# Performance work log

Hardware: AMD Instinct MI355X
Metric: run time of the kernel (lower is better)

The kernel has to match this reference:

```python
import jax, jax.numpy as jnp
import numpy as np

NA, NB, C = 50000, 50000, 128
E = 800000
S, IN, H, NBASES = 8, 64, 64, 8
NUM_LAYERS = 2
EPS = 1e-5


def setup_inputs() -> dict:
    key = jax.random.key(0)
    ks = jax.random.split(key, 16)
    inp = {
        'x_a': jax.random.normal(ks[0], (NA, C), jnp.float32),
        'x_b': jax.random.normal(ks[1], (NB, C), jnp.float32),
        'schema_x': jax.random.normal(ks[2], (S, IN), jnp.float32),
        'edge_ab': jax.random.randint(ks[3], (2, E), 0, NA, jnp.int32),
        'edge_ba': jax.random.randint(ks[4], (2, E), 0, NA, jnp.int32),
        'edge_aa': jax.random.randint(ks[5], (2, E), 0, NA, jnp.int32),
        'schema_edge_index': jax.random.randint(ks[6], (2, 24), 0, S, jnp.int32),
        'pre_W': jax.random.normal(ks[7], (H, IN), jnp.float32) * (1.0 / np.sqrt(IN)),
        'pre_b': jnp.zeros((H,), jnp.float32),
        'gcn_W': jax.random.normal(ks[8], (H, H), jnp.float32) * (1.0 / np.sqrt(H)),
        'gcn_b': jnp.zeros((H,), jnp.float32),
        'coeff_W': jax.random.normal(ks[9], (NBASES, 2 * H), jnp.float32) * (1.0 / np.sqrt(2 * H)),
        'coeff_b': jnp.zeros((NBASES,), jnp.float32),
        'bases': jax.random.normal(ks[10], (NUM_LAYERS, NBASES, C, C), jnp.float32) * (1.0 / np.sqrt(C)),
        'sage_bias': jnp.zeros((NUM_LAYERS, 3, C), jnp.float32),
        'ln_w': jnp.ones((NUM_LAYERS, 2, C), jnp.float32),
        'ln_b': jnp.zeros((NUM_LAYERS, 2, C), jnp.float32),
    }
    return inp


def _gcn_conv(x, ei, W, b):
    # PyG GCNConv: add self-loops, symmetric normalization, then linear.
    n = x.shape[0]
    loop = jnp.arange(n, dtype=ei.dtype)
    src = jnp.concatenate([ei[0], loop])
    dst = jnp.concatenate([ei[1], loop])
    deg = jax.ops.segment_sum(jnp.ones_like(dst, jnp.float32), dst, num_segments=n)
    dinv = jax.lax.rsqrt(jnp.maximum(deg, 1e-12))
    norm = dinv[src] * dinv[dst]  # [E+n]
    xw = x @ W.T  # [n, H]
    out = jax.ops.segment_sum(xw[src] * norm[:, None], dst, num_segments=n)
    return out + b


def _sage_conv(x_src, x_dst, ei, W, b):
    # PyG SAGEConv, aggr='mean': lin_l(mean_j x_src[j]) + lin_r(x_dst); lin_l.weight == lin_r.weight == W.
    n_dst = x_dst.shape[0]
    msg_sum = jax.ops.segment_sum(x_src[ei[0]], ei[1], num_segments=n_dst)
    cnt = jax.ops.segment_sum(jnp.ones(ei.shape[1], x_src.dtype), ei[1], num_segments=n_dst)
    mean = msg_sum / jnp.maximum(cnt, 1.0)[:, None]
    return (mean + x_dst) @ W.T + b


def _layer_norm(x, w, b):
    mu = jnp.mean(x, axis=-1, keepdims=True)
    var = jnp.mean(jnp.square(x - mu), axis=-1, keepdims=True)
    return (x - mu) * jax.lax.rsqrt(var + EPS) * w + b


def _edge_weight(sf_src, sf_dst, coeff_W, coeff_b, bases_l):
    combined = jnp.concatenate([sf_src, sf_dst], axis=0)  # [2H]
    coeffs = combined @ coeff_W.T + coeff_b  # [NBASES]
    return jnp.einsum('i,ijk->jk', coeffs, bases_l)  # [C, C]


def reference(x_a, x_b, schema_x, edge_ab, edge_ba, edge_aa, schema_edge_index,
              pre_W, pre_b, gcn_W, gcn_b, coeff_W, coeff_b, bases,
              sage_bias, ln_w, ln_b):
    # Schema GCN over the tiny table-level graph. table_to_index: a->0, b->1.
    h = schema_x @ pre_W.T + pre_b
    ori = h
    sf = jax.nn.relu(_gcn_conv(h, schema_edge_index, gcn_W, gcn_b))  # [S, H]

    for l in range(NUM_LAYERS):
        bases_l = bases[l]
        W_ab = _edge_weight(sf[0], sf[1], coeff_W, coeff_b, bases_l)
        W_ba = _edge_weight(sf[1], sf[0], coeff_W, coeff_b, bases_l)
        W_aa = _edge_weight(sf[0], sf[0], coeff_W, coeff_b, bases_l)
        # HeteroConv(aggr='sum'): sum SAGE outputs per destination node type.
        out_b = _sage_conv(x_a, x_b, edge_ab, W_ab, sage_bias[l, 0])
        out_a = (_sage_conv(x_b, x_a, edge_ba, W_ba, sage_bias[l, 1])
                 + _sage_conv(x_a, x_a, edge_aa, W_aa, sage_bias[l, 2]))
        x_a = jax.nn.relu(_layer_norm(out_a, ln_w[l, 0], ln_b[l, 0]))
        x_b = jax.nn.relu(_layer_norm(out_b, ln_w[l, 1], ln_b[l, 1]))

    return x_a, x_b, sf, ori
```

## Files before the change

kernel.cpp:

```cpp
#include <hip/hip_runtime.h>

#define NA 50000
#define NB 50000
#define NN 50000
#define CDIM 128
#define EDGES 800000
#define SS 8
#define INDIM 64
#define HDIM 64
#define NBASES 8
#define NBUCK 98
#define BSH 9


__device__ __forceinline__ unsigned short f2bf(float f) {
    unsigned u = __float_as_uint(f);
    return (unsigned short)((u + 0x7FFFu + ((u >> 16) & 1u)) >> 16);
}

__global__ __launch_bounds__(512) void schema_kernel(
    const float* __restrict__ schema_x, const int* __restrict__ sei,
    const float* __restrict__ preW, const float* __restrict__ preb,
    const float* __restrict__ gcnW, const float* __restrict__ gcnb,
    const float* __restrict__ coW, const float* __restrict__ cob,
    float* __restrict__ out_sf, float* __restrict__ out_ori,
    float* __restrict__ coeffs)
{
    __shared__ float h[SS][HDIM];
    __shared__ float xw[SS][HDIM];
    __shared__ float sf[SS][HDIM];
    __shared__ float deg[SS];
    __shared__ float nrm[32];
    __shared__ int es[32], ed[32];

    int t = threadIdx.x;
    int i = t >> 6, j = t & 63;

    float acc = preb[j];
    for (int k = 0; k < INDIM; k++) acc += schema_x[i * INDIM + k] * preW[j * INDIM + k];
    h[i][j] = acc;
    out_ori[i * HDIM + j] = acc;
    if (t < SS) deg[t] = 0.0f;
    __syncthreads();

    if (t < 32) {
        int s, d;
        if (t < 24) { s = sei[t]; d = sei[24 + t]; }
        else        { s = t - 24; d = t - 24; }
        es[t] = s; ed[t] = d;
        atomicAdd(&deg[d], 1.0f);
    }
    __syncthreads();
    if (t < 32) {
        nrm[t] = rsqrtf(fmaxf(deg[es[t]], 1e-12f)) * rsqrtf(fmaxf(deg[ed[t]], 1e-12f));
    }
    float a2 = 0.0f;
    for (int k = 0; k < HDIM; k++) a2 += h[i][k] * gcnW[j * HDIM + k];
    xw[i][j] = a2;
    __syncthreads();

    float o = gcnb[j];
    for (int e = 0; e < 32; e++) {
        if (ed[e] == i) o += xw[es[e]][j] * nrm[e];
    }
    float s = fmaxf(o, 0.0f);
    sf[i][j] = s;
    out_sf[i * HDIM + j] = s;
    __syncthreads();

    if (t < 24) {
        int ty = t >> 3, ii = t & 7;
        int srow = (ty == 1) ? 1 : 0;
        int drow = (ty == 0) ? 1 : 0;
        float a = cob[ii];
        for (int k = 0; k < HDIM; k++) a += sf[srow][k] * coW[ii * (2 * HDIM) + k];
        for (int k = 0; k < HDIM; k++) a += sf[drow][k] * coW[ii * (2 * HDIM) + HDIM + k];
        coeffs[ty * 8 + ii] = a;
    }
}

__global__ __launch_bounds__(256) void build_w_kernel(
    const float* __restrict__ bases, const float* __restrict__ coeffs,
    float* __restrict__ W)
{
    int idx = blockIdx.x * blockDim.x + threadIdx.x;
    int lt = idx >> 14;
    int jk = idx & 16383;
    int j = jk >> 7, k = jk & 127;
    int l = lt / 3, ty = lt % 3;
    float acc = 0.0f;
#pragma unroll
    for (int i = 0; i < NBASES; i++)
        acc += coeffs[ty * 8 + i] * bases[((size_t)(l * NBASES + i) << 14) + jk];
    W[(lt << 14) + ((k >> 2) << 9) + (j << 2) + (k & 3)] = acc;
}

__global__ __launch_bounds__(256) void tobf16_kernel(
    const float* __restrict__ in, unsigned short* __restrict__ out, int n)
{
    int i = (blockIdx.x * 256 + threadIdx.x) * 4;
    if (i >= n) return;
    float4 f = *(const float4*)(in + i);
    ushort4 o;
    o.x = f2bf(f.x); o.y = f2bf(f.y); o.z = f2bf(f.z); o.w = f2bf(f.w);
    *(ushort4*)(out + i) = o;
}

__global__ __launch_bounds__(256) void zero_rows_kernel(
    unsigned short* a0, unsigned short* b0, unsigned short* a1, unsigned short* b1)
{
    int t = threadIdx.x;
    int tab = t >> 6, w = t & 63;
    unsigned short* p = (tab == 0) ? a0 : (tab == 1) ? b0 : (tab == 2) ? a1 : b1;
    ((unsigned*)(p + (size_t)NN * CDIM))[w] = 0u;
}


__global__ __launch_bounds__(256) void bucket_count_kernel(
    const int* __restrict__ ab, const int* __restrict__ ba,
    const int* __restrict__ aa, int* __restrict__ bcnt)
{
    __shared__ int h[NBUCK];
    int t = threadIdx.x;
    int ty = blockIdx.y;
    const int* ei = (ty == 0) ? ab : (ty == 1) ? ba : aa;
    if (t < NBUCK) h[t] = 0;
    __syncthreads();
    int cb = blockIdx.x * 4096;
    int en = min(cb + 4096, EDGES);
    for (int e = cb + t; e < en; e += 256)
        atomicAdd(&h[ei[EDGES + e] >> BSH], 1);
    __syncthreads();
    if (t < NBUCK) atomicAdd(&bcnt[ty * NBUCK + t], h[t]);
}

__global__ __launch_bounds__(32) void bucket_scan_kernel(
    const int* __restrict__ bcnt, int* __restrict__ boff, int* __restrict__ bcur)
{
    int t = threadIdx.x;
    if (t < 3) {
        int run = 0;
        for (int i = 0; i < NBUCK; i++) {
            int c = bcnt[t * NBUCK + i];
            boff[t * (NBUCK + 1) + i] = run;
            bcur[t * NBUCK + i] = run;
            run += c;
        }
        boff[t * (NBUCK + 1) + NBUCK] = run;
    }
}

__global__ __launch_bounds__(256) void bucket_partition_kernel(
    const int* __restrict__ ab, const int* __restrict__ ba,
    const int* __restrict__ aa, int* __restrict__ bcur,
    unsigned* __restrict__ buf)
{
    __shared__ int h[NBUCK];
    __shared__ int basearr[NBUCK];
    __shared__ int cur[NBUCK];
    int t = threadIdx.x;
    int ty = blockIdx.y;
    const int* ei = (ty == 0) ? ab : (ty == 1) ? ba : aa;
    if (t < NBUCK) h[t] = 0;
    __syncthreads();
    int cb = blockIdx.x * 4096;
    int en = min(cb + 4096, EDGES);
    for (int e = cb + t; e < en; e += 256)
        atomicAdd(&h[ei[EDGES + e] >> BSH], 1);
    __syncthreads();
    if (t < NBUCK) {
        basearr[t] = atomicAdd(&bcur[ty * NBUCK + t], h[t]);
        cur[t] = 0;
    }
    __syncthreads();
    for (int e = cb + t; e < en; e += 256) {
        int src = ei[e], dst = ei[EDGES + e];
        int b = dst >> BSH;
        int r = atomicAdd(&cur[b], 1);
        buf[(size_t)ty * EDGES + basearr[b] + r] =
            ((unsigned)(dst & 511) << 16) | (unsigned)src;
    }
}

__global__ __launch_bounds__(256) void bucket_scatter_kernel(
    const unsigned* __restrict__ buf, const int* __restrict__ boff,
    int* __restrict__ rowptr, int* __restrict__ col)
{
    __shared__ int cnt[512];
    __shared__ int part[256];
    int t = threadIdx.x;
    int b = blockIdx.x, ty = blockIdx.y;
    int nstart = boff[ty * (NBUCK + 1) + b];
    int nend   = boff[ty * (NBUCK + 1) + b + 1];
    int n = nend - nstart;
    cnt[t] = 0; cnt[t + 256] = 0;
    __syncthreads();
    const unsigned* bb = buf + (size_t)ty * EDGES + nstart;
    for (int i = t; i < n; i += 256)
        atomicAdd(&cnt[bb[i] >> 16], 1);
    __syncthreads();
    int a0 = cnt[2 * t], a1 = cnt[2 * t + 1];
    int s = a0 + a1;
    part[t] = s;
    __syncthreads();
    for (int off = 1; off < 256; off <<= 1) {
        int v = (t >= off) ? part[t - off] : 0;
        __syncthreads();
        part[t] += v;
        __syncthreads();
    }
    int excl = part[t] - s;
    int p0 = excl, p1 = excl + a0;
    cnt[2 * t] = p0; cnt[2 * t + 1] = p1;
    int row0 = (b << BSH) + 2 * t;
    int rbase = ty * (NN + 1);
    if (row0 < NN)     rowptr[rbase + row0] = nstart + p0;
    if (row0 + 1 < NN) rowptr[rbase + row0 + 1] = nstart + p1;
    if (b == NBUCK - 1 && t == 255) rowptr[rbase + NN] = EDGES;
    __syncthreads();
    int* cc = col + (size_t)ty * EDGES + nstart;
    for (int i = t; i < n; i += 256) {
        unsigned pk = bb[i];
        int r = atomicAdd(&cnt[pk >> 16], 1);
        cc[r] = (int)(pk & 0xFFFFu);
    }
}


__device__ __forceinline__ float4 gather2_bf(
    const unsigned short* __restrict__ xsrc, const int* __restrict__ col,
    int s, int e, int half, int off)
{
    float4 g = {0.f, 0.f, 0.f, 0.f};
    int n = e - s;
    if (n > 0) {
        int cs[16];
#pragma unroll
        for (int j = 0; j < 16; j++) {
            int slot = s + 2 * j + half;
            int cc = col[min(slot, e - 1)];
            cs[j] = (slot < e) ? cc : NN;
        }
        uint2 v[16];
#pragma unroll
        for (int j = 0; j < 8; j++)
            v[j] = *(const uint2*)(xsrc + (size_t)cs[j] * CDIM + off);
        if (n > 16) {
#pragma unroll
            for (int j = 8; j < 16; j++)
                v[j] = *(const uint2*)(xsrc + (size_t)cs[j] * CDIM + off);
        } else {
#pragma unroll
            for (int j = 8; j < 16; j++) v[j] = make_uint2(0u, 0u);
        }
#pragma unroll
        for (int j = 0; j < 16; j++) {
            g.x += __uint_as_float(v[j].x << 16);
            g.y += __uint_as_float(v[j].x & 0xffff0000u);
            g.z += __uint_as_float(v[j].y << 16);
            g.w += __uint_as_float(v[j].y & 0xffff0000u);
        }
        for (int b2 = s + 32; b2 < e; b2 += 16) {
#pragma unroll
            for (int j = 0; j < 8; j++) {
                int slot = b2 + 2 * j + half;
                int cc = col[min(slot, e - 1)];
                int id = (slot < e) ? cc : NN;
                uint2 vv = *(const uint2*)(xsrc + (size_t)id * CDIM + off);
                g.x += __uint_as_float(vv.x << 16);
                g.y += __uint_as_float(vv.x & 0xffff0000u);
                g.z += __uint_as_float(vv.y << 16);
                g.w += __uint_as_float(vv.y & 0xffff0000u);
            }
        }
    }
    g.x += __shfl_xor(g.x, 32, 64);
    g.y += __shfl_xor(g.y, 32, 64);
    g.z += __shfl_xor(g.z, 32, 64);
    g.w += __shfl_xor(g.w, 32, 64);
    return g;
}

__global__ __launch_bounds__(128) void fuse_b_kernel(
    const unsigned short* __restrict__ xsrc, const float* __restrict__ xdst,
    const int* __restrict__ rowptr, const int* __restrict__ col,
    const float* __restrict__ W, const float* __restrict__ bias,
    const float* __restrict__ lnw, const float* __restrict__ lnb,
    float* __restrict__ xnext, unsigned short* __restrict__ xnext_bf)
{
    const int R = 8;
    __shared__ __align__(16) float U[R][CDIM];
    int t = threadIdx.x;
    int base = blockIdx.x * R;
    int wv = t >> 6;
    int lane = t & 63;
    int half = lane >> 5, cl = lane & 31;
    int off = cl << 2;

    for (int rr = 0; rr < R / 2; rr++) {
        int r = rr * 2 + wv;
        int row = base + r;
        int s = rowptr[row], e = rowptr[row + 1];
        float4 g = gather2_bf(xsrc, col, s, e, half, off);
        if (half == 0) {
            float inv = 1.0f / (float)max(e - s, 1);
            float4 xv = *(const float4*)(xdst + (size_t)row * CDIM + off);
            float4 u;
            u.x = g.x * inv + xv.x; u.y = g.y * inv + xv.y;
            u.z = g.z * inv + xv.z; u.w = g.w * inv + xv.w;
            *(float4*)&U[r][off] = u;
        }
    }
    __syncthreads();

    float acc[R];
    float b = bias[t];
#pragma unroll
    for (int r = 0; r < R; r++) acc[r] = b;

    const float4* Wp4 = (const float4*)W;
    for (int k4 = 0; k4 < 32; k4++) {
        float4 w = Wp4[k4 * 128 + t];
#pragma unroll
        for (int r = 0; r < R; r++) {
            float4 u = *(const float4*)&U[r][k4 * 4];
            acc[r] += u.x * w.x + u.y * w.y + u.z * w.z + u.w * w.w;
        }
    }

    __syncthreads();
#pragma unroll
    for (int r = 0; r < R; r++) U[r][t] = acc[r];
    __syncthreads();

    float lw0 = lnw[lane], lw1 = lnw[lane + 64];
    float lb0 = lnb[lane], lb1 = lnb[lane + 64];
    for (int rr = 0; rr < R / 2; rr++) {
        int r = rr * 2 + wv;
        int row = base + r;
        float v0 = U[r][lane], v1 = U[r][lane + 64];
        float s = v0 + v1, s2 = v0 * v0 + v1 * v1;
#pragma unroll
        for (int o2 = 32; o2 > 0; o2 >>= 1) {
            s  += __shfl_xor(s,  o2, 64);
            s2 += __shfl_xor(s2, o2, 64);
        }
        float mu = s * (1.0f / CDIM);
        float var = s2 * (1.0f / CDIM) - mu * mu;
        float rs = rsqrtf(var + 1e-5f);
        float o0 = fmaxf((v0 - mu) * rs * lw0 + lb0, 0.0f);
        float o1 = fmaxf((v1 - mu) * rs * lw1 + lb1, 0.0f);
        size_t oi = (size_t)row * CDIM;
        xnext[oi + lane] = o0;
        xnext[oi + lane + 64] = o1;
        if (xnext_bf) {
            xnext_bf[oi + lane] = f2bf(o0);
            xnext_bf[oi + lane + 64] = f2bf(o1);
        }
    }
}

__global__ __launch_bounds__(128) void fuse_a_kernel(
    const unsigned short* __restrict__ xsrc1, const int* __restrict__ rowptr1, const int* __restrict__ col1,
    const unsigned short* __restrict__ xsrc2, const int* __restrict__ rowptr2, const int* __restrict__ col2,
    const float* __restrict__ xdst,
    const float* __restrict__ W1, const float* __restrict__ W2,
    const float* __restrict__ bias1, const float* __restrict__ bias2,
    const float* __restrict__ lnw, const float* __restrict__ lnb,
    float* __restrict__ xnext, unsigned short* __restrict__ xnext_bf)
{
    const int R = 8;
    __shared__ __align__(16) float U[R][CDIM];
    __shared__ __align__(16) float V[R][CDIM];
    int t = threadIdx.x;
    int base = blockIdx.x * R;
    int wv = t >> 6;
    int lane = t & 63;
    int half = lane >> 5, cl = lane & 31;
    int off = cl << 2;

    for (int rr = 0; rr < R / 2; rr++) {
        int r = rr * 2 + wv;
        int row = base + r;
        int s1 = rowptr1[row], e1 = rowptr1[row + 1];
        float4 g1 = gather2_bf(xsrc1, col1, s1, e1, half, off);
        int s2 = rowptr2[row], e2 = rowptr2[row + 1];
        float4 g2 = gather2_bf(xsrc2, col2, s2, e2, half, off);
        if (half == 0) {
            float4 xv = *(const float4*)(xdst + (size_t)row * CDIM + off);
            float i1 = 1.0f / (float)max(e1 - s1, 1);
            float i2 = 1.0f / (float)max(e2 - s2, 1);
            float4 u, v;
            u.x = g1.x * i1 + xv.x; u.y = g1.y * i1 + xv.y;
            u.z = g1.z * i1 + xv.z; u.w = g1.w * i1 + xv.w;
            v.x = g2.x * i2 + xv.x; v.y = g2.y * i2 + xv.y;
            v.z = g2.z * i2 + xv.z; v.w = g2.w * i2 + xv.w;
            *(float4*)&U[r][off] = u;
            *(float4*)&V[r][off] = v;
        }
    }
    __syncthreads();

    float acc[R];
    float b = bias1[t] + bias2[t];
#pragma unroll
    for (int r = 0; r < R; r++) acc[r] = b;

    const float4* W1p = (const float4*)W1;
    const float4* W2p = (const float4*)W2;
    for (int k4 = 0; k4 < 32; k4++) {
        float4 w1 = W1p[k4 * 128 + t];
        float4 w2 = W2p[k4 * 128 + t];
#pragma unroll
        for (int r = 0; r < R; r++) {
            float4 u = *(const float4*)&U[r][k4 * 4];
            float4 v = *(const float4*)&V[r][k4 * 4];
            acc[r] += u.x * w1.x + u.y * w1.y + u.z * w1.z + u.w * w1.w
                    + v.x * w2.x + v.y * w2.y + v.z * w2.z + v.w * w2.w;
        }
    }

    __syncthreads();
#pragma unroll
    for (int r = 0; r < R; r++) U[r][t] = acc[r];
    __syncthreads();

    float lw0 = lnw[lane], lw1 = lnw[lane + 64];
    float lb0 = lnb[lane], lb1 = lnb[lane + 64];
    for (int rr = 0; rr < R / 2; rr++) {
        int r = rr * 2 + wv;
        int row = base + r;
        float v0 = U[r][lane], v1 = U[r][lane + 64];
        float s = v0 + v1, s2 = v0 * v0 + v1 * v1;
#pragma unroll
        for (int o2 = 32; o2 > 0; o2 >>= 1) {
            s  += __shfl_xor(s,  o2, 64);
            s2 += __shfl_xor(s2, o2, 64);
        }
        float mu = s * (1.0f / CDIM);
        float var = s2 * (1.0f / CDIM) - mu * mu;
        float rs = rsqrtf(var + 1e-5f);
        float o0 = fmaxf((v0 - mu) * rs * lw0 + lb0, 0.0f);
        float o1 = fmaxf((v1 - mu) * rs * lw1 + lb1, 0.0f);
        size_t oi = (size_t)row * CDIM;
        xnext[oi + lane] = o0;
        xnext[oi + lane + 64] = o1;
        if (xnext_bf) {
            xnext_bf[oi + lane] = f2bf(o0);
            xnext_bf[oi + lane + 64] = f2bf(o1);
        }
    }
}

extern "C" void kernel_launch(void* const* d_in, const int* in_sizes, int n_in,
                              void* d_out, int out_size, void* d_ws, size_t ws_size,
                              hipStream_t stream)
{
    const float* x_a      = (const float*)d_in[0];
    const float* x_b      = (const float*)d_in[1];
    const float* schema_x = (const float*)d_in[2];
    const int*   e_ab     = (const int*)d_in[3];
    const int*   e_ba     = (const int*)d_in[4];
    const int*   e_aa     = (const int*)d_in[5];
    const int*   sei      = (const int*)d_in[6];
    const float* preW     = (const float*)d_in[7];
    const float* preb     = (const float*)d_in[8];
    const float* gcnW     = (const float*)d_in[9];
    const float* gcnb     = (const float*)d_in[10];
    const float* coW      = (const float*)d_in[11];
    const float* cob      = (const float*)d_in[12];
    const float* bases    = (const float*)d_in[13];
    const float* sbias    = (const float*)d_in[14];
    const float* lnw      = (const float*)d_in[15];
    const float* lnb      = (const float*)d_in[16];

    float* out     = (float*)d_out;
    float* out_xa  = out;
    float* out_xb  = out + 6400000;
    float* out_sf  = out + 12800000;
    float* out_ori = out + 12800512;

    float* ws = (float*)d_ws;
    int*      col    = (int*)ws;
    int*      rowptr = (int*)(ws + 2400000);
    unsigned* buf    = (unsigned*)(ws + 2550016);
    int*      bcnt   = (int*)(ws + 4950016);
    int*      boff   = (int*)(ws + 4950320);
    int*      bcur   = (int*)(ws + 4950624);
    float* xa_buf = ws + 4950928;
    float* xb_buf = ws + 11350928;
    float* Wbuf   = ws + 17750928;
    float* coeffs = ws + 17849232;
    unsigned short* xa_bf0 = (unsigned short*)(ws + 17849264);
    unsigned short* xb_bf0 = (unsigned short*)(ws + 21049328);
    unsigned short* xa_bf1 = (unsigned short*)(ws + 24249392);
    unsigned short* xb_bf1 = (unsigned short*)(ws + 27449456);

    schema_kernel<<<1, 512, 0, stream>>>(schema_x, sei, preW, preb, gcnW, gcnb,
                                         coW, cob, out_sf, out_ori, coeffs);
    build_w_kernel<<<384, 256, 0, stream>>>(bases, coeffs, Wbuf);

    tobf16_kernel<<<(NA * CDIM / 4 + 255) / 256, 256, 0, stream>>>(x_a, xa_bf0, NA * CDIM);
    tobf16_kernel<<<(NB * CDIM / 4 + 255) / 256, 256, 0, stream>>>(x_b, xb_bf0, NB * CDIM);
    zero_rows_kernel<<<1, 256, 0, stream>>>(xa_bf0, xb_bf0, xa_bf1, xb_bf1);

    hipMemsetAsync(bcnt, 0, 3 * NBUCK * sizeof(int), stream);
    dim3 cgrid((EDGES + 4095) / 4096, 3);
    bucket_count_kernel<<<cgrid, 256, 0, stream>>>(e_ab, e_ba, e_aa, bcnt);
    bucket_scan_kernel<<<1, 32, 0, stream>>>(bcnt, boff, bcur);
    bucket_partition_kernel<<<cgrid, 256, 0, stream>>>(e_ab, e_ba, e_aa, bcur, buf);
    dim3 sgrid(NBUCK, 3);
    bucket_scatter_kernel<<<sgrid, 256, 0, stream>>>(buf, boff, rowptr, col);

    const int* rp_ab = rowptr;
    const int* rp_ba = rowptr + (NN + 1);
    const int* rp_aa = rowptr + 2 * (NN + 1);
    const int* col_ab = col;
    const int* col_ba = col + EDGES;
    const int* col_aa = col + 2 * EDGES;

    for (int l = 0; l < 2; l++) {
        const float* xa_cur = (l == 0) ? x_a : xa_buf;
        const float* xb_cur = (l == 0) ? x_b : xb_buf;
        const unsigned short* xa_bf = (l == 0) ? xa_bf0 : xa_bf1;
        const unsigned short* xb_bf = (l == 0) ? xb_bf0 : xb_bf1;
        const float* Wab = Wbuf + (size_t)(l * 3 + 0) * 16384;
        const float* Wba = Wbuf + (size_t)(l * 3 + 1) * 16384;
        const float* Waa = Wbuf + (size_t)(l * 3 + 2) * 16384;
        float* xa_nxt = (l == 0) ? xa_buf : out_xa;
        float* xb_nxt = (l == 0) ? xb_buf : out_xb;
        unsigned short* xa_nbf = (l == 0) ? xa_bf1 : nullptr;
        unsigned short* xb_nbf = (l == 0) ? xb_bf1 : nullptr;

        fuse_b_kernel<<<NB / 8, 128, 0, stream>>>(
            xa_bf, xb_cur, rp_ab, col_ab, Wab,
            sbias + (size_t)(l * 3 + 0) * 128,
            lnw + (size_t)(l * 2 + 1) * 128, lnb + (size_t)(l * 2 + 1) * 128,
            xb_nxt, xb_nbf);
        fuse_a_kernel<<<NA / 8, 128, 0, stream>>>(
            xb_bf, rp_ba, col_ba, xa_bf, rp_aa, col_aa, xa_cur,
            Wba, Waa,
            sbias + (size_t)(l * 3 + 1) * 128, sbias + (size_t)(l * 3 + 2) * 128,
            lnw + (size_t)(l * 2 + 0) * 128, lnb + (size_t)(l * 2 + 0) * 128,
            xa_nxt, xa_nbf);
    }
}
```

Measured before the change: 657.3 us.

## Use bf16 MFMA for SAGE linear transforms with larger row tiles

Replaces the scalar FP32 dot-product GEMM in the fused SAGE kernels with bf16 MFMA 16x16x32 instructions. Aggregated rows are staged in LDS as bf16, and the edge weights are built directly in bf16 row-major form. Blocks now cover 32 rows with 256 threads, with bounds checks for the ragged final block. This cuts ALU time in the transform step, but rounding both operands to bf16 adds precision error, and the kernels are likely gather-bound anyway.

```diff
diff --git a/kernel.cpp b/kernel.cpp
--- a/kernel.cpp
+++ b/kernel.cpp
@@ -12,6 +12,9 @@
 #define NBUCK 98
 #define BSH 9
 
+typedef __attribute__((ext_vector_type(8))) short bf16x8;
+typedef __attribute__((ext_vector_type(4))) float f32x4;
+
 
 __device__ __forceinline__ unsigned short f2bf(float f) {
     unsigned u = __float_as_uint(f);
@@ -81,18 +84,17 @@
 
 __global__ __launch_bounds__(256) void build_w_kernel(
     const float* __restrict__ bases, const float* __restrict__ coeffs,
-    float* __restrict__ W)
+    unsigned short* __restrict__ Wbf)
 {
     int idx = blockIdx.x * blockDim.x + threadIdx.x;
     int lt = idx >> 14;
     int jk = idx & 16383;
-    int j = jk >> 7, k = jk & 127;
     int l = lt / 3, ty = lt % 3;
     float acc = 0.0f;
 #pragma unroll
     for (int i = 0; i < NBASES; i++)
         acc += coeffs[ty * 8 + i] * bases[((size_t)(l * NBASES + i) << 14) + jk];
-    W[(lt << 14) + ((k >> 2) << 9) + (j << 2) + (k & 3)] = acc;
+    Wbf[idx] = f2bf(acc);
 }
 
 __global__ __launch_bounds__(256) void tobf16_kernel(
@@ -281,64 +283,86 @@
     return g;
 }
 
-__global__ __launch_bounds__(128) void fuse_b_kernel(
+#define RROWS 32
+#define USTR 136
+#define SSTR 129
+
+__global__ __launch_bounds__(256) void fuse_b_kernel(
     const unsigned short* __restrict__ xsrc, const float* __restrict__ xdst,
     const int* __restrict__ rowptr, const int* __restrict__ col,
-    const float* __restrict__ W, const float* __restrict__ bias,
+    const unsigned short* __restrict__ Wbf, const float* __restrict__ bias,
     const float* __restrict__ lnw, const float* __restrict__ lnb,
     float* __restrict__ xnext, unsigned short* __restrict__ xnext_bf)
 {
-    const int R = 8;
-    __shared__ __align__(16) float U[R][CDIM];
-    int t = threadIdx.x;
-    int base = blockIdx.x * R;
+    __shared__ unsigned short Ubf[RROWS * USTR];
+    __shared__ float stage[RROWS * SSTR];
+    int t = threadIdx.x;
+    int base = blockIdx.x * RROWS;
     int wv = t >> 6;
     int lane = t & 63;
     int half = lane >> 5, cl = lane & 31;
     int off = cl << 2;
 
-    for (int rr = 0; rr < R / 2; rr++) {
-        int r = rr * 2 + wv;
+    for (int rr = 0; rr < RROWS / 4; rr++) {
+        int r = rr * 4 + wv;
         int row = base + r;
-        int s = rowptr[row], e = rowptr[row + 1];
-        float4 g = gather2_bf(xsrc, col, s, e, half, off);
-        if (half == 0) {
-            float inv = 1.0f / (float)max(e - s, 1);
-            float4 xv = *(const float4*)(xdst + (size_t)row * CDIM + off);
-            float4 u;
-            u.x = g.x * inv + xv.x; u.y = g.y * inv + xv.y;
-            u.z = g.z * inv + xv.z; u.w = g.w * inv + xv.w;
-            *(float4*)&U[r][off] = u;
-        }
-    }
-    __syncthreads();
-
-    float acc[R];
-    float b = bias[t];
-#pragma unroll
-    for (int r = 0; r < R; r++) acc[r] = b;
-
-    const float4* Wp4 = (const float4*)W;
-    for (int k4 = 0; k4 < 32; k4++) {
-        float4 w = Wp4[k4 * 128 + t];
-#pragma unroll
-        for (int r = 0; r < R; r++) {
-            float4 u = *(const float4*)&U[r][k4 * 4];
-            acc[r] += u.x * w.x + u.y * w.y + u.z * w.z + u.w * w.w;
-        }
-    }
-
-    __syncthreads();
-#pragma unroll
-    for (int r = 0; r < R; r++) U[r][t] = acc[r];
-    __syncthreads();
-
+        if (row < NN) {
+            int s = rowptr[row], e = rowptr[row + 1];
+            float4 g = gather2_bf(xsrc, col, s, e, half, off);
+            if (half == 0) {
+                float inv = 1.0f / (float)max(e - s, 1);
+                const float4 xv = *(const float4*)(xdst + (size_t)row * CDIM + off);
+                ushort4 o;
+                o.x = f2bf(g.x * inv + xv.x);
+                o.y = f2bf(g.y * inv + xv.y);
+                o.z = f2bf(g.z * inv + xv.z);
+                o.w = f2bf(g.w * inv + xv.w);
+                *(ushort4*)&Ubf[r * USTR + off] = o;
+            }
+        } else if (half == 0) {
+            *(ushort4*)&Ubf[r * USTR + off] = make_ushort4(0, 0, 0, 0);
+        }
+    }
+    __syncthreads();
+
+    int qd = lane >> 4;
+    int ln16 = lane & 15;
+    f32x4 acc00 = {0.f,0.f,0.f,0.f}, acc01 = acc00, acc10 = acc00, acc11 = acc00;
+#pragma unroll
+    for (int ks = 0; ks < 4; ks++) {
+        int koff = ks * 32 + qd * 8;
+        bf16x8 a0 = *(const bf16x8*)&Ubf[(ln16) * USTR + koff];
+        bf16x8 a1 = *(const bf16x8*)&Ubf[(16 + ln16) * USTR + koff];
+        bf16x8 b0 = *(const bf16x8*)&Wbf[(size_t)((2 * wv + 0) * 16 + ln16) * CDIM + koff];
+        bf16x8 b1 = *(const bf16x8*)&Wbf[(size_t)((2 * wv + 1) * 16 + ln16) * CDIM + koff];
+        acc00 = __builtin_amdgcn_mfma_f32_16x16x32_bf16(a0, b0, acc00, 0, 0, 0);
+        acc01 = __builtin_amdgcn_mfma_f32_16x16x32_bf16(a0, b1, acc01, 0, 0, 0);
+        acc10 = __builtin_amdgcn_mfma_f32_16x16x32_bf16(a1, b0, acc10, 0, 0, 0);
+        acc11 = __builtin_amdgcn_mfma_f32_16x16x32_bf16(a1, b1, acc11, 0, 0, 0);
+    }
+    {
+        int c0 = (2 * wv + 0) * 16 + ln16;
+        int c1 = (2 * wv + 1) * 16 + ln16;
+#pragma unroll
+        for (int i = 0; i < 4; i++) {
+            int r0 = qd * 4 + i;
+            stage[r0 * SSTR + c0] = acc00[i];
+            stage[r0 * SSTR + c1] = acc01[i];
+            stage[(16 + r0) * SSTR + c0] = acc10[i];
+            stage[(16 + r0) * SSTR + c1] = acc11[i];
+        }
+    }
+    __syncthreads();
+
+    float b0v = bias[lane], b1v = bias[lane + 64];
     float lw0 = lnw[lane], lw1 = lnw[lane + 64];
     float lb0 = lnb[lane], lb1 = lnb[lane + 64];
-    for (int rr = 0; rr < R / 2; rr++) {
-        int r = rr * 2 + wv;
+    for (int rr = 0; rr < RROWS / 4; rr++) {
+        int r = rr * 4 + wv;
         int row = base + r;
-        float v0 = U[r][lane], v1 = U[r][lane + 64];
+        if (row >= NN) continue;
+        float v0 = stage[r * SSTR + lane] + b0v;
+        float v1 = stage[r * SSTR + lane + 64] + b1v;
         float s = v0 + v1, s2 = v0 * v0 + v1 * v1;
 #pragma unroll
         for (int o2 = 32; o2 > 0; o2 >>= 1) {
@@ -360,77 +384,101 @@
     }
 }
 
-__global__ __launch_bounds__(128) void fuse_a_kernel(
+__global__ __launch_bounds__(256) void fuse_a_kernel(
     const unsigned short* __restrict__ xsrc1, const int* __restrict__ rowptr1, const int* __restrict__ col1,
     const unsigned short* __restrict__ xsrc2, const int* __restrict__ rowptr2, const int* __restrict__ col2,
     const float* __restrict__ xdst,
-    const float* __restrict__ W1, const float* __restrict__ W2,
+    const unsigned short* __restrict__ W1bf, const unsigned short* __restrict__ W2bf,
     const float* __restrict__ bias1, const float* __restrict__ bias2,
     const float* __restrict__ lnw, const float* __restrict__ lnb,
     float* __restrict__ xnext, unsigned short* __restrict__ xnext_bf)
 {
-    const int R = 8;
-    __shared__ __align__(16) float U[R][CDIM];
-    __shared__ __align__(16) float V[R][CDIM];
-    int t = threadIdx.x;
-    int base = blockIdx.x * R;
+    __shared__ unsigned short Ubf[RROWS * USTR];
+    __shared__ unsigned short Vbf[RROWS * USTR];
+    __shared__ float stage[RROWS * SSTR];
+    int t = threadIdx.x;
+    int base = blockIdx.x * RROWS;
     int wv = t >> 6;
     int lane = t & 63;
     int half = lane >> 5, cl = lane & 31;
     int off = cl << 2;
 
-    for (int rr = 0; rr < R / 2; rr++) {
-        int r = rr * 2 + wv;
+    for (int rr = 0; rr < RROWS / 4; rr++) {
+        int r = rr * 4 + wv;
         int row = base + r;
-        int s1 = rowptr1[row], e1 = rowptr1[row + 1];
-        float4 g1 = gather2_bf(xsrc1, col1, s1, e1, half, off);
-        int s2 = rowptr2[row], e2 = rowptr2[row + 1];
-        float4 g2 = gather2_bf(xsrc2, col2, s2, e2, half, off);
-        if (half == 0) {
-            float4 xv = *(const float4*)(xdst + (size_t)row * CDIM + off);
-            float i1 = 1.0f / (float)max(e1 - s1, 1);
-            float i2 = 1.0f / (float)max(e2 - s2, 1);
-            float4 u, v;
-            u.x = g1.x * i1 + xv.x; u.y = g1.y * i1 + xv.y;
-            u.z = g1.z * i1 + xv.z; u.w = g1.w * i1 + xv.w;
-            v.x = g2.x * i2 + xv.x; v.y = g2.y * i2 + xv.y;
-            v.z = g2.z * i2 + xv.z; v.w = g2.w * i2 + xv.w;
-            *(float4*)&U[r][off] = u;
-            *(float4*)&V[r][off] = v;
-        }
-    }
-    __syncthreads();
-
-    float acc[R];
-    float b = bias1[t] + bias2[t];
-#pragma unroll
-    for (int r = 0; r < R; r++) acc[r] = b;
-
-    const float4* W1p = (const float4*)W1;
-    const float4* W2p = (const float4*)W2;
-    for (int k4 = 0; k4 < 32; k4++) {
-        float4 w1 = W1p[k4 * 128 + t];
-        float4 w2 = W2p[k4 * 128 + t];
-#pragma unroll
-        for (int r = 0; r < R; r++) {
-            float4 u = *(const float4*)&U[r][k4 * 4];
-            float4 v = *(const float4*)&V[r][k4 * 4];
-            acc[r] += u.x * w1.x + u.y * w1.y + u.z * w1.z + u.w * w1.w
-                    + v.x * w2.x + v.y * w2.y + v.z * w2.z + v.w * w2.w;
-        }
-    }
-
-    __syncthreads();
-#pragma unroll
-    for (int r = 0; r < R; r++) U[r][t] = acc[r];
-    __syncthreads();
-
+        if (row < NN) {
+            int s1 = rowptr1[row], e1 = rowptr1[row + 1];
+            float4 g1 = gather2_bf(xsrc1, col1, s1, e1, half, off);
+            int s2 = rowptr2[row], e2 = rowptr2[row + 1];
+            float4 g2 = gather2_bf(xsrc2, col2, s2, e2, half, off);
+            if (half == 0) {
+                const float4 xv = *(const float4*)(xdst + (size_t)row * CDIM + off);
+                float i1 = 1.0f / (float)max(e1 - s1, 1);
+                float i2 = 1.0f / (float)max(e2 - s2, 1);
+                ushort4 ou, ov;
+                ou.x = f2bf(g1.x * i1 + xv.x); ou.y = f2bf(g1.y * i1 + xv.y);
+                ou.z = f2bf(g1.z * i1 + xv.z); ou.w = f2bf(g1.w * i1 + xv.w);
+                ov.x = f2bf(g2.x * i2 + xv.x); ov.y = f2bf(g2.y * i2 + xv.y);
+                ov.z = f2bf(g2.z * i2 + xv.z); ov.w = f2bf(g2.w * i2 + xv.w);
+                *(ushort4*)&Ubf[r * USTR + off] = ou;
+                *(ushort4*)&Vbf[r * USTR + off] = ov;
+            }
+        } else if (half == 0) {
+            *(ushort4*)&Ubf[r * USTR + off] = make_ushort4(0, 0, 0, 0);
+            *(ushort4*)&Vbf[r * USTR + off] = make_ushort4(0, 0, 0, 0);
+        }
+    }
+    __syncthreads();
+
+    int qd = lane >> 4;
+    int ln16 = lane & 15;
+    f32x4 acc00 = {0.f,0.f,0.f,0.f}, acc01 = acc00, acc10 = acc00, acc11 = acc00;
+#pragma unroll
+    for (int ks = 0; ks < 4; ks++) {
+        int koff = ks * 32 + qd * 8;
+        bf16x8 aU0 = *(const bf16x8*)&Ubf[(ln16) * USTR + koff];
+        bf16x8 aU1 = *(const bf16x8*)&Ubf[(16 + ln16) * USTR + koff];
+        bf16x8 aV0 = *(const bf16x8*)&Vbf[(ln16) * USTR + koff];
+        bf16x8 aV1 = *(const bf16x8*)&Vbf[(16 + ln16) * USTR + koff];
+        size_t wrow0 = (size_t)((2 * wv + 0) * 16 + ln16) * CDIM + koff;
+        size_t wrow1 = (size_t)((2 * wv + 1) * 16 + ln16) * CDIM + koff;
+        bf16x8 b10 = *(const bf16x8*)&W1bf[wrow0];
+        bf16x8 b11 = *(const bf16x8*)&W1bf[wrow1];
+        bf16x8 b20 = *(const bf16x8*)&W2bf[wrow0];
+        bf16x8 b21 = *(const bf16x8*)&W2bf[wrow1];
+        acc00 = __builtin_amdgcn_mfma_f32_16x16x32_bf16(aU0, b10, acc00, 0, 0, 0);
+        acc01 = __builtin_amdgcn_mfma_f32_16x16x32_bf16(aU0, b11, acc01, 0, 0, 0);
+        acc10 = __builtin_amdgcn_mfma_f32_16x16x32_bf16(aU1, b10, acc10, 0, 0, 0);
+        acc11 = __builtin_amdgcn_mfma_f32_16x16x32_bf16(aU1, b11, acc11, 0, 0, 0);
+        acc00 = __builtin_amdgcn_mfma_f32_16x16x32_bf16(aV0, b20, acc00, 0, 0, 0);
+        acc01 = __builtin_amdgcn_mfma_f32_16x16x32_bf16(aV0, b21, acc01, 0, 0, 0);
+        acc10 = __builtin_amdgcn_mfma_f32_16x16x32_bf16(aV1, b20, acc10, 0, 0, 0);
+        acc11 = __builtin_amdgcn_mfma_f32_16x16x32_bf16(aV1, b21, acc11, 0, 0, 0);
+    }
+    {
+        int c0 = (2 * wv + 0) * 16 + ln16;
+        int c1 = (2 * wv + 1) * 16 + ln16;
+#pragma unroll
+        for (int i = 0; i < 4; i++) {
+            int r0 = qd * 4 + i;
+            stage[r0 * SSTR + c0] = acc00[i];
+            stage[r0 * SSTR + c1] = acc01[i];
+            stage[(16 + r0) * SSTR + c0] = acc10[i];
+            stage[(16 + r0) * SSTR + c1] = acc11[i];
+        }
+    }
+    __syncthreads();
+
+    float b0v = bias1[lane] + bias2[lane];
+    float b1v = bias1[lane + 64] + bias2[lane + 64];
     float lw0 = lnw[lane], lw1 = lnw[lane + 64];
     float lb0 = lnb[lane], lb1 = lnb[lane + 64];
-    for (int rr = 0; rr < R / 2; rr++) {
-        int r = rr * 2 + wv;
+    for (int rr = 0; rr < RROWS / 4; rr++) {
+        int r = rr * 4 + wv;
         int row = base + r;
-        float v0 = U[r][lane], v1 = U[r][lane + 64];
+        if (row >= NN) continue;
+        float v0 = stage[r * SSTR + lane] + b0v;
+        float v1 = stage[r * SSTR + lane + 64] + b1v;
         float s = v0 + v1, s2 = v0 * v0 + v1 * v1;
 #pragma unroll
         for (int o2 = 32; o2 > 0; o2 >>= 1) {
@@ -489,16 +537,16 @@
     int*      bcur   = (int*)(ws + 4950624);
     float* xa_buf = ws + 4950928;
     float* xb_buf = ws + 11350928;
-    float* Wbuf   = ws + 17750928;
-    float* coeffs = ws + 17849232;
-    unsigned short* xa_bf0 = (unsigned short*)(ws + 17849264);
-    unsigned short* xb_bf0 = (unsigned short*)(ws + 21049328);
-    unsigned short* xa_bf1 = (unsigned short*)(ws + 24249392);
-    unsigned short* xb_bf1 = (unsigned short*)(ws + 27449456);
+    unsigned short* Wbf = (unsigned short*)(ws + 17750928);
+    float* coeffs = ws + 17800080;
+    unsigned short* xa_bf0 = (unsigned short*)(ws + 17800112);
+    unsigned short* xb_bf0 = (unsigned short*)(ws + 21000176);
+    unsigned short* xa_bf1 = (unsigned short*)(ws + 24200240);
+    unsigned short* xb_bf1 = (unsigned short*)(ws + 27400304);
 
     schema_kernel<<<1, 512, 0, stream>>>(schema_x, sei, preW, preb, gcnW, gcnb,
                                          coW, cob, out_sf, out_ori, coeffs);
-    build_w_kernel<<<384, 256, 0, stream>>>(bases, coeffs, Wbuf);
+    build_w_kernel<<<384, 256, 0, stream>>>(bases, coeffs, Wbf);
 
     tobf16_kernel<<<(NA * CDIM / 4 + 255) / 256, 256, 0, stream>>>(x_a, xa_bf0, NA * CDIM);
     tobf16_kernel<<<(NB * CDIM / 4 + 255) / 256, 256, 0, stream>>>(x_b, xb_bf0, NB * CDIM);
@@ -519,25 +567,27 @@
     const int* col_ba = col + EDGES;
     const int* col_aa = col + 2 * EDGES;
 
+    const int fgrid = (NN + RROWS - 1) / RROWS;
+
     for (int l = 0; l < 2; l++) {
         const float* xa_cur = (l == 0) ? x_a : xa_buf;
         const float* xb_cur = (l == 0) ? x_b : xb_buf;
         const unsigned short* xa_bf = (l == 0) ? xa_bf0 : xa_bf1;
         const unsigned short* xb_bf = (l == 0) ? xb_bf0 : xb_bf1;
-        const float* Wab = Wbuf + (size_t)(l * 3 + 0) * 16384;
-        const float* Wba = Wbuf + (size_t)(l * 3 + 1) * 16384;
-        const float* Waa = Wbuf + (size_t)(l * 3 + 2) * 16384;
+        const unsigned short* Wab = Wbf + (size_t)(l * 3 + 0) * 16384;
+        const unsigned short* Wba = Wbf + (size_t)(l * 3 + 1) * 16384;
+        const unsigned short* Waa = Wbf + (size_t)(l * 3 + 2) * 16384;
         float* xa_nxt = (l == 0) ? xa_buf : out_xa;
         float* xb_nxt = (l == 0) ? xb_buf : out_xb;
         unsigned short* xa_nbf = (l == 0) ? xa_bf1 : nullptr;
         unsigned short* xb_nbf = (l == 0) ? xb_bf1 : nullptr;
 
-        fuse_b_kernel<<<NB / 8, 128, 0, stream>>>(
+        fuse_b_kernel<<<fgrid, 256, 0, stream>>>(
             xa_bf, xb_cur, rp_ab, col_ab, Wab,
             sbias + (size_t)(l * 3 + 0) * 128,
             lnw + (size_t)(l * 2 + 1) * 128, lnb + (size_t)(l * 2 + 1) * 128,
             xb_nxt, xb_nbf);
-        fuse_a_kernel<<<NA / 8, 128, 0, stream>>>(
+        fuse_a_kernel<<<fgrid, 256, 0, stream>>>(
             xb_bf, rp_ba, col_ba, xa_bf, rp_aa, col_aa, xa_cur,
             Wba, Waa,
             sbias + (size_t)(l * 3 + 1) * 128, sbias + (size_t)(l * 3 + 2) * 128,
```

Result: faster. 558.2 us (-15.1%).
